# Optimization experiments

Measured on AMD Instinct MI355X. Metric: run time of the kernel, lower is better.

Reference implementation:

```python
import jax, jax.numpy as jnp
import numpy as np

COLUMN_COUNT = 2048
CELLS_PER_COLUMN = 32
NUM_CELLS = COLUMN_COUNT * CELLS_PER_COLUMN
MAX_SEGMENTS = 16
MAX_SYNAPSES = 32
ACTIVATION_THRESHOLD = 13
PERMANENCE_CONNECTED = 0.5


def setup_inputs() -> dict:
    key = jax.random.key(0)
    k1, k2, k3, k4, k5 = jax.random.split(key, 5)
    active_columns = jax.random.randint(k1, (COLUMN_COUNT,), 0, 2).astype(jnp.float32)
    prev_active = jax.random.randint(k2, (NUM_CELLS,), 0, 2).astype(jnp.float32)
    prev_predictive = jax.random.randint(k3, (NUM_CELLS,), 0, 2).astype(jnp.float32)
    seg_pre = jax.random.randint(k4, (NUM_CELLS, MAX_SEGMENTS, MAX_SYNAPSES), 0, NUM_CELLS, dtype=jnp.int32)
    seg_perm = jax.random.uniform(k5, (NUM_CELLS, MAX_SEGMENTS, MAX_SYNAPSES), dtype=jnp.float32)
    return {
        'active_columns': active_columns,
        'prev_active': prev_active,
        'prev_predictive': prev_predictive,
        'seg_pre': seg_pre,
        'seg_perm': seg_perm,
    }


def _best_segment_activity(seg_pre, connected, active_vec):
    """Per cell: max over segments of (# synapses that are connected AND whose
    presynaptic cell is active). Mirrors _get_segment_activity/_get_best_matching_segment."""
    pre_active = active_vec[seg_pre] > 0          # [N, S, K] irregular gather
    counts = jnp.sum(connected & pre_active, axis=-1)  # [N, S]
    return jnp.max(counts, axis=-1)               # [N]


def reference(active_columns, prev_active, prev_predictive, seg_pre, seg_perm):
    C, cpc = COLUMN_COUNT, CELLS_PER_COLUMN
    connected = seg_perm >= PERMANENCE_CONNECTED   # [N, S, K]

    col_active = active_columns > 0                           # [C]
    pred = (prev_predictive > 0).reshape(C, cpc)              # [C, cpc]
    col_has_pred = jnp.any(pred, axis=1)                      # [C]

    # Active cells: predicted cells if any prediction in column, else burst (all cells).
    new_active = jnp.where(col_active[:, None],
                           jnp.where(col_has_pred[:, None], pred, True),
                           False)                             # [C, cpc]
    active_flat = new_active.reshape(-1).astype(jnp.float32)  # [N]

    # New predictive cells: any segment with activity >= activation_threshold
    # w.r.t. the NEW active set.
    best_act = _best_segment_activity(seg_pre, connected, active_flat)  # [N]
    new_predictive = (best_act >= ACTIVATION_THRESHOLD).astype(jnp.float32)

    # Anomaly: fraction of active columns with no predicted cell.
    n_active_cols = jnp.sum(col_active)
    n_predicted = jnp.sum(col_active & col_has_pred)
    anomaly = (1.0 - n_predicted / jnp.maximum(n_active_cols, 1)).astype(jnp.float32)

    return active_flat, new_predictive, anomaly


if __name__ == '__main__':
    out = reference(**setup_inputs())
    print([o.shape for o in out])
```

## Files before the change

### kernel.cpp

```cpp
#include <hip/hip_runtime.h>

#define COLS    2048
#define CPC     32
#define NCELLS  65536
#define SEGS    16
#define SYN     32
#define THRESH  13

#define CELLS_PER_BLOCK 16
#define PREDICT_GRID (NCELLS / CELLS_PER_BLOCK)

__global__ __launch_bounds__(256) void tm_active_kernel(
    const float* __restrict__ active_columns,
    const float* __restrict__ prev_predictive,
    float* __restrict__ out_active,
    unsigned int* __restrict__ ws_mask,
    int* __restrict__ ws_cnt)
{
    int n = blockIdx.x * 256 + threadIdx.x;
    int c = n >> 5;
    int j = n & 31;
    int lane = threadIdx.x & 63;

    bool predbit    = prev_predictive[n] > 0.0f;
    bool col_active = active_columns[c] > 0.0f;

    unsigned long long pb = __ballot(predbit);
    unsigned int colmask = (lane < 32) ? (unsigned int)pb : (unsigned int)(pb >> 32);
    bool has_pred = (colmask != 0u);

    bool active = col_active && (has_pred ? predbit : true);
    out_active[n] = active ? 1.0f : 0.0f;

    unsigned long long ab = __ballot(active);
    if (lane == 0)  ws_mask[c] = (unsigned int)ab;
    if (lane == 32) ws_mask[c] = (unsigned int)(ab >> 32);

    bool rep = (j == 0);
    unsigned long long aa = __ballot(rep && col_active);
    unsigned long long pp = __ballot(rep && col_active && has_pred);
    if (lane == 0) {
        atomicAdd(&ws_cnt[0], __popcll(aa));
        atomicAdd(&ws_cnt[1], __popcll(pp));
    }
}

__global__ __launch_bounds__(256, 2) void tm_predict_kernel(
    const int*   __restrict__ seg_pre,
    const float* __restrict__ seg_perm,
    const unsigned int* __restrict__ ws_mask,
    const int*   __restrict__ ws_cnt,
    float* __restrict__ out_pred,
    float* __restrict__ out_anomaly)
{
    __shared__ unsigned int mask[COLS];
    int tid = threadIdx.x;
    #pragma unroll
    for (int i = 0; i < COLS / 256; ++i)
        mask[tid + 256 * i] = ws_mask[tid + 256 * i];
    __syncthreads();

    int wave = tid >> 6;
    int lane = tid & 63;
    int cell0 = blockIdx.x * CELLS_PER_BLOCK + wave * 4;

    const int4*   pre4  = (const int4*)  seg_pre  + (size_t)cell0 * 128;
    const float4* perm4 = (const float4*)seg_perm + (size_t)cell0 * 128;

    int4   P[8];
    float4 Q[8];
    #pragma unroll
    for (int c = 0; c < 4; ++c) {
        P[2 * c]     = pre4 [c * 128 + lane];
        P[2 * c + 1] = pre4 [c * 128 + lane + 64];
        Q[2 * c]     = perm4[c * 128 + lane];
        Q[2 * c + 1] = perm4[c * 128 + lane + 64];
    }

    #pragma unroll
    for (int c = 0; c < 4; ++c) {
        int4   p0 = P[2 * c],     p1 = P[2 * c + 1];
        float4 q0 = Q[2 * c],     q1 = Q[2 * c + 1];

        int c0 = 0, c1 = 0;
        c0 += (q0.x >= 0.5f && ((mask[(unsigned)p0.x >> 5] >> ((unsigned)p0.x & 31u)) & 1u)) ? 1 : 0;
        c0 += (q0.y >= 0.5f && ((mask[(unsigned)p0.y >> 5] >> ((unsigned)p0.y & 31u)) & 1u)) ? 1 : 0;
        c0 += (q0.z >= 0.5f && ((mask[(unsigned)p0.z >> 5] >> ((unsigned)p0.z & 31u)) & 1u)) ? 1 : 0;
        c0 += (q0.w >= 0.5f && ((mask[(unsigned)p0.w >> 5] >> ((unsigned)p0.w & 31u)) & 1u)) ? 1 : 0;
        c1 += (q1.x >= 0.5f && ((mask[(unsigned)p1.x >> 5] >> ((unsigned)p1.x & 31u)) & 1u)) ? 1 : 0;
        c1 += (q1.y >= 0.5f && ((mask[(unsigned)p1.y >> 5] >> ((unsigned)p1.y & 31u)) & 1u)) ? 1 : 0;
        c1 += (q1.z >= 0.5f && ((mask[(unsigned)p1.z >> 5] >> ((unsigned)p1.z & 31u)) & 1u)) ? 1 : 0;
        c1 += (q1.w >= 0.5f && ((mask[(unsigned)p1.w >> 5] >> ((unsigned)p1.w & 31u)) & 1u)) ? 1 : 0;

        int v = c0 | (c1 << 16);
        v += __shfl_xor(v, 1, 64);
        v += __shfl_xor(v, 2, 64);
        v += __shfl_xor(v, 4, 64);
        int m = max(v & 0xffff, v >> 16);
        m = max(m, __shfl_xor(m, 8, 64));
        m = max(m, __shfl_xor(m, 16, 64));
        m = max(m, __shfl_xor(m, 32, 64));

        if (lane == 0)
            out_pred[cell0 + c] = (m >= THRESH) ? 1.0f : 0.0f;
    }

    if (blockIdx.x == 0 && tid == 0) {
        int na = ws_cnt[0];
        int np = ws_cnt[1];
        *out_anomaly = 1.0f - (float)np / (float)(na > 1 ? na : 1);
    }
}

extern "C" void kernel_launch(void* const* d_in, const int* in_sizes, int n_in,
                              void* d_out, int out_size, void* d_ws, size_t ws_size,
                              hipStream_t stream) {
    const float* active_columns  = (const float*)d_in[0];
    const float* prev_predictive = (const float*)d_in[2];
    const int*   seg_pre         = (const int*)d_in[3];
    const float* seg_perm        = (const float*)d_in[4];
    float* out = (float*)d_out;

    unsigned int* ws_mask = (unsigned int*)d_ws;
    int* ws_cnt = (int*)((char*)d_ws + COLS * sizeof(unsigned int));

    hipMemsetAsync(ws_cnt, 0, 2 * sizeof(int), stream);

    tm_active_kernel<<<NCELLS / 256, 256, 0, stream>>>(
        active_columns, prev_predictive, out, ws_mask, ws_cnt);

    tm_predict_kernel<<<PREDICT_GRID, 256, 0, stream>>>(
        seg_pre, seg_perm, ws_mask, ws_cnt,
        out + NCELLS, out + 2 * NCELLS);
}
```

Measured before the change: 313.2 us.

## Replace atomic anomaly counters with per-column flags reduced in predict kernel

The active kernel now writes a per-column byte flag (active, active-and-predicted) instead of doing global atomicAdds, which removes the hipMemsetAsync launch and the atomic contention. Block 0 of the predict kernel reduces these 2048 flags with wave shuffles and shared memory to compute the anomaly. The change also drops the occupancy hint from the predict kernel's launch bounds and adds a scheduling barrier after the bulk loads. Block 0 takes on extra reduction work, and the looser launch bounds may change register allocation.

```diff
diff --git a/kernel.cpp b/kernel.cpp
--- a/kernel.cpp
+++ b/kernel.cpp
@@ -15,7 +15,7 @@
     const float* __restrict__ prev_predictive,
     float* __restrict__ out_active,
     unsigned int* __restrict__ ws_mask,
-    int* __restrict__ ws_cnt)
+    unsigned char* __restrict__ ws_flags)
 {
     int n = blockIdx.x * 256 + threadIdx.x;
     int c = n >> 5;
@@ -36,24 +36,21 @@
     if (lane == 0)  ws_mask[c] = (unsigned int)ab;
     if (lane == 32) ws_mask[c] = (unsigned int)(ab >> 32);
 
-    bool rep = (j == 0);
-    unsigned long long aa = __ballot(rep && col_active);
-    unsigned long long pp = __ballot(rep && col_active && has_pred);
-    if (lane == 0) {
-        atomicAdd(&ws_cnt[0], __popcll(aa));
-        atomicAdd(&ws_cnt[1], __popcll(pp));
-    }
+    if (j == 0)
+        ws_flags[c] = (unsigned char)((col_active ? 1 : 0) |
+                                      ((col_active && has_pred) ? 2 : 0));
 }
 
-__global__ __launch_bounds__(256, 2) void tm_predict_kernel(
+__global__ __launch_bounds__(256) void tm_predict_kernel(
     const int*   __restrict__ seg_pre,
     const float* __restrict__ seg_perm,
     const unsigned int* __restrict__ ws_mask,
-    const int*   __restrict__ ws_cnt,
+    const unsigned char* __restrict__ ws_flags,
     float* __restrict__ out_pred,
     float* __restrict__ out_anomaly)
 {
     __shared__ unsigned int mask[COLS];
+    __shared__ int red[4];
     int tid = threadIdx.x;
     #pragma unroll
     for (int i = 0; i < COLS / 256; ++i)
@@ -76,6 +73,7 @@
         Q[2 * c]     = perm4[c * 128 + lane];
         Q[2 * c + 1] = perm4[c * 128 + lane + 64];
     }
+    __builtin_amdgcn_sched_barrier(0);
 
     #pragma unroll
     for (int c = 0; c < 4; ++c) {
@@ -105,10 +103,28 @@
             out_pred[cell0 + c] = (m >= THRESH) ? 1.0f : 0.0f;
     }
 
-    if (blockIdx.x == 0 && tid == 0) {
-        int na = ws_cnt[0];
-        int np = ws_cnt[1];
-        *out_anomaly = 1.0f - (float)np / (float)(na > 1 ? na : 1);
+    if (blockIdx.x == 0) {
+        int na = 0, np = 0;
+        #pragma unroll
+        for (int i = 0; i < COLS / 256; ++i) {
+            unsigned f = ws_flags[tid * (COLS / 256) + i];
+            na += (f & 1);
+            np += ((f >> 1) & 1);
+        }
+        int v = na | (np << 16);
+        v += __shfl_xor(v, 1, 64);
+        v += __shfl_xor(v, 2, 64);
+        v += __shfl_xor(v, 4, 64);
+        v += __shfl_xor(v, 8, 64);
+        v += __shfl_xor(v, 16, 64);
+        v += __shfl_xor(v, 32, 64);
+        if (lane == 0) red[wave] = v;
+        __syncthreads();
+        if (tid == 0) {
+            int t = red[0] + red[1] + red[2] + red[3];
+            int NA = t & 0xffff, NP = t >> 16;
+            *out_anomaly = 1.0f - (float)NP / (float)(NA > 1 ? NA : 1);
+        }
     }
 }
 
@@ -121,15 +137,13 @@
     const float* seg_perm        = (const float*)d_in[4];
     float* out = (float*)d_out;
 
-    unsigned int* ws_mask = (unsigned int*)d_ws;
-    int* ws_cnt = (int*)((char*)d_ws + COLS * sizeof(unsigned int));
-
-    hipMemsetAsync(ws_cnt, 0, 2 * sizeof(int), stream);
+    unsigned int*  ws_mask  = (unsigned int*)d_ws;
+    unsigned char* ws_flags = (unsigned char*)d_ws + COLS * sizeof(unsigned int);
 
     tm_active_kernel<<<NCELLS / 256, 256, 0, stream>>>(
-        active_columns, prev_predictive, out, ws_mask, ws_cnt);
+        active_columns, prev_predictive, out, ws_mask, ws_flags);
 
     tm_predict_kernel<<<PREDICT_GRID, 256, 0, stream>>>(
-        seg_pre, seg_perm, ws_mask, ws_cnt,
+        seg_pre, seg_perm, ws_mask, ws_flags,
         out + NCELLS, out + 2 * NCELLS);
 }
```

Result: faster. 286.0 us (-8.7%).
